# Kernel tuning notes

Hardware: AMD Instinct MI355X
Metric: run time of the kernel (lower is better)

Reference implementation:

```python
import jax, jax.numpy as jnp
import numpy as np

N = 50000        # nodes
E = 250000       # edges (first N are self-loops -> every node has in-degree >= 1)
H = 12           # num_heads
D = 64           # per-head dim (in_dim == out_dim == 64)
NEG_SLOPE = 0.2  # LeakyReLU alpha


def setup_inputs() -> dict:
    key = jax.random.key(0)
    k1, k2, k3, k4, k5, k6, k7 = jax.random.split(key, 7)
    h = jax.random.normal(k1, (N, H * D), dtype=jnp.float32)
    # self-loops + random in-neighbors so segment softmax is well defined for all dst
    src = jnp.concatenate([jnp.arange(N, dtype=jnp.int32),
                           jax.random.randint(k2, (E - N,), 0, N, dtype=jnp.int32)])
    dst = jnp.concatenate([jnp.arange(N, dtype=jnp.int32),
                           jax.random.randint(k3, (E - N,), 0, N, dtype=jnp.int32)])
    xav = 1.414 / np.sqrt(D)  # ~ xavier_normal gain=1.414
    W_fc = jax.random.normal(k4, (D, D), dtype=jnp.float32) * xav
    attn_l = jax.random.normal(k5, (H, D), dtype=jnp.float32) * 0.15
    attn_r = jax.random.normal(k6, (H, D), dtype=jnp.float32) * 0.15
    W_res = jax.random.normal(k7, (D, D), dtype=jnp.float32) * xav
    return {"h": h, "W_fc": W_fc, "attn_l": attn_l, "attn_r": attn_r,
            "W_res": W_res, "src": src, "dst": dst}


def reference(h, W_fc, attn_l, attn_r, W_res, src, dst):
    n = h.shape[0]
    hh = h.reshape(n, H, D)                              # [N,H,D]
    # fc is Linear(D, D, bias=False) shared across heads: y = x @ W^T
    ft = jnp.einsum('nhd,ed->nhe', hh, W_fc)             # [N,H,D]
    a1 = jnp.einsum('nhd,hd->nh', ft, attn_l)            # [N,H]
    a2 = jnp.einsum('nhd,hd->nh', ft, attn_r)            # [N,H]
    # edge_attention: leaky_relu(src.a1 + dst.a2)
    e = jax.nn.leaky_relu(a1[src] + a2[dst], negative_slope=NEG_SLOPE)  # [E,H]
    # segment softmax over incoming edges per destination node (stable)
    m = jax.ops.segment_max(e, dst, num_segments=n)       # [N,H]
    ee = jnp.exp(e - m[dst])                              # [E,H]
    denom = jax.ops.segment_sum(ee, dst, num_segments=n)  # [N,H]
    alpha = ee / denom[dst]                               # [E,H]
    # message: alpha * src ft, scatter-sum into dst
    agg = jax.ops.segment_sum(alpha[:, :, None] * ft[src], dst, num_segments=n)  # [N,H,D]
    # residual: res_fc(h) per head, then ReLU(flatten)
    res = jnp.einsum('nhd,ed->nhe', hh, W_res)            # [N,H,D]
    return jax.nn.relu((res + agg).reshape(n, H * D))     # [N,768]
```

## Files before the change

### kernel.cpp

```cpp
#include <hip/hip_runtime.h>
#include <hip/hip_bf16.h>

#define N_NODES 50000
#define N_EDGES 250000
#define NHEAD   12
#define NH      (N_NODES * NHEAD)
#define ROW_TILES (NH / 16)

typedef __bf16 bf16_t;
typedef __bf16 bf16x8 __attribute__((ext_vector_type(8)));
typedef __bf16 bf16x4 __attribute__((ext_vector_type(4)));
typedef float  f32x4  __attribute__((ext_vector_type(4)));

__device__ __forceinline__ bf16x8 cvt8(f32x4 a, f32x4 b) {
    bf16x8 r;
    r[0] = (bf16_t)a[0]; r[1] = (bf16_t)a[1]; r[2] = (bf16_t)a[2]; r[3] = (bf16_t)a[3];
    r[4] = (bf16_t)b[0]; r[5] = (bf16_t)b[1]; r[6] = (bf16_t)b[2]; r[7] = (bf16_t)b[3];
    return r;
}

__global__ __launch_bounds__(256) void k_deg_prep(
    const int* __restrict__ dst, int* __restrict__ deg,
    const float* __restrict__ wfc, const float* __restrict__ wres,
    const float* __restrict__ attl, const float* __restrict__ attr,
    bf16_t* __restrict__ wfb, bf16_t* __restrict__ wrb,
    bf16_t* __restrict__ ulb, bf16_t* __restrict__ urb)
{
    int b = blockIdx.x;
    if (b < 245) {
        int i4 = b * 256 + threadIdx.x;
        if (i4 < N_EDGES / 4) {
            int4 q = reinterpret_cast<const int4*>(dst)[i4];
            atomicAdd(&deg[q.x], 1);
            atomicAdd(&deg[q.y], 1);
            atomicAdd(&deg[q.z], 1);
            atomicAdd(&deg[q.w], 1);
        }
    } else if (b < 261) {
        int t = (b - 245) * 256 + threadIdx.x;
        wfb[t] = (bf16_t)wfc[t];
        wrb[t] = (bf16_t)wres[t];
    } else if (b < 265) {
        int u = (b - 261) * 256 + threadIdx.x;
        int hh = u >> 6, d = u & 63;
        float s = 0.f;
        if (hh < NHEAD) {
#pragma unroll 8
            for (int e = 0; e < 64; ++e) s += attl[hh * 64 + e] * wfc[e * 64 + d];
        }
        ulb[u] = (bf16_t)s;
    } else {
        int u = (b - 265) * 256 + threadIdx.x;
        int hh = u >> 6, d = u & 63;
        float s = 0.f;
        if (hh < NHEAD) {
#pragma unroll 8
            for (int e = 0; e < 64; ++e) s += attr[hh * 64 + e] * wfc[e * 64 + d];
        }
        urb[u] = (bf16_t)s;
    }
}

__global__ __launch_bounds__(1024) void k_scan(const int* __restrict__ deg,
                                               int* __restrict__ cursor) {
    __shared__ int s[1024];
    const int CH = 52;
    int t = threadIdx.x;
    int base = t * CH;
    int loc[CH];
    if (base + CH <= N_NODES) {
        const int4* p = reinterpret_cast<const int4*>(deg + base);
#pragma unroll
        for (int i = 0; i < CH / 4; ++i) {
            int4 q = p[i];
            loc[4 * i + 0] = q.x; loc[4 * i + 1] = q.y;
            loc[4 * i + 2] = q.z; loc[4 * i + 3] = q.w;
        }
    } else {
#pragma unroll
        for (int i = 0; i < CH; ++i) {
            int idx = base + i;
            loc[i] = (idx < N_NODES) ? deg[idx] : 0;
        }
    }
    int sum = 0;
#pragma unroll
    for (int i = 0; i < CH; ++i) sum += loc[i];
    s[t] = sum;
    __syncthreads();
    for (int off = 1; off < 1024; off <<= 1) {
        int v = (t >= off) ? s[t - off] : 0;
        __syncthreads();
        s[t] += v;
        __syncthreads();
    }
    int run = s[t] - sum;
#pragma unroll
    for (int i = 0; i < CH; ++i) {
        int idx = base + i;
        if (idx < N_NODES) {
            cursor[idx] = run;
            run += loc[i];
        }
    }
}

__global__ __launch_bounds__(256) void k_fill_gemm(
    const int* __restrict__ src, const int* __restrict__ dst,
    int* __restrict__ cursor, int* __restrict__ csr_src,
    const float* __restrict__ h,
    const bf16_t* __restrict__ wfb,
    const bf16_t* __restrict__ wrb,
    const bf16_t* __restrict__ ulb,
    const bf16_t* __restrict__ urb,
    bf16_t* __restrict__ ft,
    bf16_t* __restrict__ resb,
    float* __restrict__ al,
    float* __restrict__ ar)
{
    __shared__ bf16_t sb[4][2][16 * 72];
    if (blockIdx.x >= 1875) {
        int i = (blockIdx.x - 1875) * 256 + threadIdx.x;
        if (i < N_EDGES) {
            int d = dst[i];
            int pos = atomicAdd(&cursor[d], 1);
            csr_src[pos] = src[i];
        }
        return;
    }
    int bid  = blockIdx.x;
    int wv   = threadIdx.x >> 6;
    int lane = threadIdx.x & 63;
    int lr = lane & 15, lg = lane >> 4;
    int l8 = lane & 7,  lrow = lane >> 3;
    bf16_t* fs = &sb[wv][0][0];
    bf16_t* rs = &sb[wv][1][0];

    const f32x4*  hv  = reinterpret_cast<const f32x4*>(h);
    const bf16x8* wf  = reinterpret_cast<const bf16x8*>(wfb);
    const bf16x8* wr  = reinterpret_cast<const bf16x8*>(wrb);
    const bf16x8* ulv = reinterpret_cast<const bf16x8*>(ulb);
    const bf16x8* urv = reinterpret_cast<const bf16x8*>(urb);
    bf16x8 ul0 = ulv[lr * 8 + lg], ul1 = ulv[lr * 8 + 4 + lg];
    bf16x8 ur0 = urv[lr * 8 + lg], ur1 = urv[lr * 8 + 4 + lg];

    const int nw = 1875 * 4;
    int tile = bid * 4 + wv;

    f32x4 c0, c1, c2, c3;
    if (tile < ROW_TILES) {
        int ab = (tile * 16 + lr) * 16 + lg * 2;
        c0 = __builtin_nontemporal_load(hv + ab);
        c1 = __builtin_nontemporal_load(hv + ab + 1);
        c2 = __builtin_nontemporal_load(hv + ab + 8);
        c3 = __builtin_nontemporal_load(hv + ab + 9);
    }
    while (tile < ROW_TILES) {
        int nxt = tile + nw;
        f32x4 n0, n1, n2, n3;
        if (nxt < ROW_TILES) {
            int ab = (nxt * 16 + lr) * 16 + lg * 2;
            n0 = __builtin_nontemporal_load(hv + ab);
            n1 = __builtin_nontemporal_load(hv + ab + 1);
            n2 = __builtin_nontemporal_load(hv + ab + 8);
            n3 = __builtin_nontemporal_load(hv + ab + 9);
        }
        bf16x8 a0 = cvt8(c0, c1), a1 = cvt8(c2, c3);
        int r0 = tile << 4;
        int r  = r0 + lr;
        int hh = r % NHEAD;

        f32x4 dl = {0.f, 0.f, 0.f, 0.f}, dr = {0.f, 0.f, 0.f, 0.f};
        dl = __builtin_amdgcn_mfma_f32_16x16x32_bf16(ul0, a0, dl, 0, 0, 0);
        dl = __builtin_amdgcn_mfma_f32_16x16x32_bf16(ul1, a1, dl, 0, 0, 0);
        dr = __builtin_amdgcn_mfma_f32_16x16x32_bf16(ur0, a0, dr, 0, 0, 0);
        dr = __builtin_amdgcn_mfma_f32_16x16x32_bf16(ur1, a1, dr, 0, 0, 0);
        if (lg == (hh >> 2)) {
#pragma unroll
            for (int j = 0; j < 4; ++j)
                if ((hh & 3) == j) { al[r] = dl[j]; ar[r] = dr[j]; }
        }

#pragma unroll
        for (int nt = 0; nt < 4; ++nt) {
            int brow = (nt * 16 + lr) * 8;
            f32x4 z = {0.f, 0.f, 0.f, 0.f};
            z = __builtin_amdgcn_mfma_f32_16x16x32_bf16(wf[brow + lg],     a0, z, 0, 0, 0);
            z = __builtin_amdgcn_mfma_f32_16x16x32_bf16(wf[brow + 4 + lg], a1, z, 0, 0, 0);
            f32x4 y = {0.f, 0.f, 0.f, 0.f};
            y = __builtin_amdgcn_mfma_f32_16x16x32_bf16(wr[brow + lg],     a0, y, 0, 0, 0);
            y = __builtin_amdgcn_mfma_f32_16x16x32_bf16(wr[brow + 4 + lg], a1, y, 0, 0, 0);
            bf16x4 pf, pe;
#pragma unroll
            for (int j = 0; j < 4; ++j) { pf[j] = (bf16_t)z[j]; pe[j] = (bf16_t)y[j]; }
            *reinterpret_cast<bf16x4*>(fs + lr * 72 + nt * 16 + lg * 4) = pf;
            *reinterpret_cast<bf16x4*>(rs + lr * 72 + nt * 16 + lg * 4) = pe;
        }

#pragma unroll
        for (int k = 0; k < 2; ++k) {
            int row = lrow + k * 8;
            bf16x8 vf = *reinterpret_cast<const bf16x8*>(fs + row * 72 + l8 * 8);
            bf16x8 vr = *reinterpret_cast<const bf16x8*>(rs + row * 72 + l8 * 8);
            *reinterpret_cast<bf16x8*>(ft   + (r0 + row) * 64 + l8 * 8) = vf;
            *reinterpret_cast<bf16x8*>(resb + (r0 + row) * 64 + l8 * 8) = vr;
        }

        c0 = n0; c1 = n1; c2 = n2; c3 = n3;
        tile = nxt;
    }
}

#define DB 8
__global__ __launch_bounds__(256) void k_agg(
    const int* __restrict__ cur, const int* __restrict__ csr_src,
    const float* __restrict__ al, const float* __restrict__ ar,
    const bf16_t* __restrict__ ft, const bf16_t* __restrict__ resb,
    float* __restrict__ out)
{
    int d0 = (blockIdx.x * 256 + threadIdx.x) >> 6;
    d0 = __builtin_amdgcn_readfirstlane(d0);
    if (d0 >= N_NODES) return;
    int l  = threadIdx.x & 63;
    int hA = l >> 3;
    int hB = 8 + (l >> 4);
    int u_l = l / 12;
    int h_l = l - u_l * 12;
    int beg = d0 ? cur[d0 - 1] : 0;
    int end = cur[d0];
    float arW = 0.f;
    if (l < 48) arW = ar[d0 * NHEAD + h_l];

    float accA[8] = {0,0,0,0,0,0,0,0};
    float accB[4] = {0,0,0,0};
    float denA = 0.f, denB = 0.f;

    for (int j0 = beg; j0 < end; j0 += DB) {
        int idx[DB];
#pragma unroll
        for (int u = 0; u < DB; ++u) {
            int j = j0 + u;
            idx[u] = csr_src[(j < end) ? j : beg];
        }
        float wv0 = 0.f, wv1 = 0.f;
        {
            int e0 = idx[0], e1 = idx[4];
            e0 = (u_l == 1) ? idx[1] : e0;  e1 = (u_l == 1) ? idx[5] : e1;
            e0 = (u_l == 2) ? idx[2] : e0;  e1 = (u_l == 2) ? idx[6] : e1;
            e0 = (u_l == 3) ? idx[3] : e0;  e1 = (u_l == 3) ? idx[7] : e1;
            if (l < 48) {
                float x0 = al[e0 * NHEAD + h_l] + arW;
                float x1 = al[e1 * NHEAD + h_l] + arW;
                x0 = (x0 > 0.f) ? x0 : 0.2f * x0;
                x1 = (x1 > 0.f) ? x1 : 0.2f * x1;
                wv0 = ((j0 + u_l)     < end) ? __expf(x0) : 0.f;
                wv1 = ((j0 + 4 + u_l) < end) ? __expf(x1) : 0.f;
            }
        }
        float wA[DB], wB[DB];
#pragma unroll
        for (int u = 0; u < 4; ++u) {
            wA[u]     = __shfl(wv0, u * 12 + hA, 64);
            wB[u]     = __shfl(wv0, u * 12 + hB, 64);
            wA[u + 4] = __shfl(wv1, u * 12 + hA, 64);
            wB[u + 4] = __shfl(wv1, u * 12 + hB, 64);
        }
        bf16x8 vA[DB]; bf16x4 vB[DB];
#pragma unroll
        for (int u = 0; u < DB; ++u) {
            const bf16_t* row = ft + idx[u] * 768;
            vA[u] = *reinterpret_cast<const bf16x8*>(row + 8 * l);
            vB[u] = *reinterpret_cast<const bf16x4*>(row + 512 + 4 * l);
        }
#pragma unroll
        for (int u = 0; u < DB; ++u) {
            denA += wA[u]; denB += wB[u];
#pragma unroll
            for (int k = 0; k < 8; ++k) accA[k] += wA[u] * (float)vA[u][k];
#pragma unroll
            for (int k = 0; k < 4; ++k) accB[k] += wB[u] * (float)vB[u][k];
        }
    }

    const bf16_t* rrow = resb + d0 * 768;
    bf16x8 rA = __builtin_nontemporal_load(reinterpret_cast<const bf16x8*>(rrow + 8 * l));
    bf16x4 rB = __builtin_nontemporal_load(reinterpret_cast<const bf16x4*>(rrow + 512 + 4 * l));
    float* orow = out + d0 * 768;
    f32x4 o0, o1, o2;
    float ia = 1.f / denA, ib = 1.f / denB;
#pragma unroll
    for (int k = 0; k < 4; ++k) {
        float x = (float)rA[k] + accA[k] * ia;         o0[k] = x > 0.f ? x : 0.f;
        float y = (float)rA[k + 4] + accA[k + 4] * ia; o1[k] = y > 0.f ? y : 0.f;
        float z = (float)rB[k] + accB[k] * ib;         o2[k] = z > 0.f ? z : 0.f;
    }
    __builtin_nontemporal_store(o0, reinterpret_cast<f32x4*>(orow + 8 * l));
    __builtin_nontemporal_store(o1, reinterpret_cast<f32x4*>(orow + 8 * l + 4));
    __builtin_nontemporal_store(o2, reinterpret_cast<f32x4*>(orow + 512 + 4 * l));
}

extern "C" void kernel_launch(void* const* d_in, const int* in_sizes, int n_in,
                              void* d_out, int out_size, void* d_ws, size_t ws_size,
                              hipStream_t stream) {
    const float* h    = (const float*)d_in[0];
    const float* wfc  = (const float*)d_in[1];
    const float* attl = (const float*)d_in[2];
    const float* attr = (const float*)d_in[3];
    const float* wres = (const float*)d_in[4];
    const int*   src  = (const int*)d_in[5];
    const int*   dst  = (const int*)d_in[6];
    float* out = (float*)d_out;

    char* ws = (char*)d_ws;
    bf16_t* ft     = (bf16_t*)(ws + 0);
    bf16_t* resb   = (bf16_t*)(ws + 76800000);
    float*  al     = (float*)(ws + 153600000);
    float*  ar     = (float*)(ws + 156000000);
    int*    deg    = (int*)(ws + 158400000);
    int*    cursor = (int*)(ws + 158800896);
    int*    csrsrc = (int*)(ws + 159001344);
    bf16_t* wfb    = (bf16_t*)(ws + 160001344);
    bf16_t* wrb    = (bf16_t*)(ws + 160009536);
    bf16_t* ulb    = (bf16_t*)(ws + 160017728);
    bf16_t* urb    = (bf16_t*)(ws + 160019776);

    (void)hipMemsetAsync(deg, 0, N_NODES * sizeof(int), stream);
    k_deg_prep<<<269, 256, 0, stream>>>(dst, deg, wfc, wres, attl, attr, wfb, wrb, ulb, urb);
    k_scan<<<1, 1024, 0, stream>>>(deg, cursor);
    k_fill_gemm<<<1875 + 977, 256, 0, stream>>>(src, dst, cursor, csrsrc,
                                                h, wfb, wrb, ulb, urb, ft, resb, al, ar);
    k_agg<<<(N_NODES + 3) / 4, 256, 0, stream>>>(cursor, csrsrc, al, ar, ft, resb, out);
}
```

Baseline: 209.6 us.

## Interleave fill and GEMM blocks and deepen h prefetch to two tiles

The CSR fill blocks are now interleaved with GEMM blocks (every third block id) instead of all running after the GEMM blocks, so the atomic scatter overlaps with the streaming GEMM. The GEMM block count changes, and the register prefetch of h goes from one tile ahead to two. Nontemporal loads become ordinary loads. This aims to hide memory latency and balance work across CUs, at the cost of more live registers and a different cache policy for h.

```diff
diff --git a/kernel.cpp b/kernel.cpp
--- a/kernel.cpp
+++ b/kernel.cpp
@@ -6,6 +6,8 @@
 #define NHEAD   12
 #define NH      (N_NODES * NHEAD)
 #define ROW_TILES (NH / 16)
+#define NGEMMB  1954
+#define NFILLB  977
 
 typedef __bf16 bf16_t;
 typedef __bf16 bf16x8 __attribute__((ext_vector_type(8)));
@@ -119,8 +121,9 @@
     float* __restrict__ ar)
 {
     __shared__ bf16_t sb[4][2][16 * 72];
-    if (blockIdx.x >= 1875) {
-        int i = (blockIdx.x - 1875) * 256 + threadIdx.x;
+    int bid = blockIdx.x;
+    if (bid % 3 == 2) {
+        int i = (bid / 3) * 256 + threadIdx.x;
         if (i < N_EDGES) {
             int d = dst[i];
             int pos = atomicAdd(&cursor[d], 1);
@@ -128,7 +131,7 @@
         }
         return;
     }
-    int bid  = blockIdx.x;
+    int gid  = (bid / 3) * 2 + (bid % 3);
     int wv   = threadIdx.x >> 6;
     int lane = threadIdx.x & 63;
     int lr = lane & 15, lg = lane >> 4;
@@ -144,26 +147,28 @@
     bf16x8 ul0 = ulv[lr * 8 + lg], ul1 = ulv[lr * 8 + 4 + lg];
     bf16x8 ur0 = urv[lr * 8 + lg], ur1 = urv[lr * 8 + 4 + lg];
 
-    const int nw = 1875 * 4;
-    int tile = bid * 4 + wv;
-
-    f32x4 c0, c1, c2, c3;
+    const int nw = NGEMMB * 4;
+    int tile = gid * 4 + wv;
+    int t1 = tile + nw;
+
+    f32x4 c0, c1, c2, c3, d0_, d1_, d2_, d3_;
     if (tile < ROW_TILES) {
         int ab = (tile * 16 + lr) * 16 + lg * 2;
-        c0 = __builtin_nontemporal_load(hv + ab);
-        c1 = __builtin_nontemporal_load(hv + ab + 1);
-        c2 = __builtin_nontemporal_load(hv + ab + 8);
-        c3 = __builtin_nontemporal_load(hv + ab + 9);
+        c0 = hv[ab];     c1 = hv[ab + 1];
+        c2 = hv[ab + 8]; c3 = hv[ab + 9];
+    }
+    if (t1 < ROW_TILES) {
+        int ab = (t1 * 16 + lr) * 16 + lg * 2;
+        d0_ = hv[ab];     d1_ = hv[ab + 1];
+        d2_ = hv[ab + 8]; d3_ = hv[ab + 9];
     }
     while (tile < ROW_TILES) {
-        int nxt = tile + nw;
-        f32x4 n0, n1, n2, n3;
-        if (nxt < ROW_TILES) {
-            int ab = (nxt * 16 + lr) * 16 + lg * 2;
-            n0 = __builtin_nontemporal_load(hv + ab);
-            n1 = __builtin_nontemporal_load(hv + ab + 1);
-            n2 = __builtin_nontemporal_load(hv + ab + 8);
-            n3 = __builtin_nontemporal_load(hv + ab + 9);
+        int t2 = t1 + nw;
+        f32x4 e0, e1, e2, e3;
+        if (t2 < ROW_TILES) {
+            int ab = (t2 * 16 + lr) * 16 + lg * 2;
+            e0 = hv[ab];     e1 = hv[ab + 1];
+            e2 = hv[ab + 8]; e3 = hv[ab + 9];
         }
         bf16x8 a0 = cvt8(c0, c1), a1 = cvt8(c2, c3);
         int r0 = tile << 4;
@@ -206,8 +211,9 @@
             *reinterpret_cast<bf16x8*>(resb + (r0 + row) * 64 + l8 * 8) = vr;
         }
 
-        c0 = n0; c1 = n1; c2 = n2; c3 = n3;
-        tile = nxt;
+        c0 = d0_; c1 = d1_; c2 = d2_; c3 = d3_;
+        d0_ = e0; d1_ = e1; d2_ = e2; d3_ = e3;
+        tile = t1; t1 = t2;
     }
 }
 
@@ -327,7 +333,7 @@
     (void)hipMemsetAsync(deg, 0, N_NODES * sizeof(int), stream);
     k_deg_prep<<<269, 256, 0, stream>>>(dst, deg, wfc, wres, attl, attr, wfb, wrb, ulb, urb);
     k_scan<<<1, 1024, 0, stream>>>(deg, cursor);
-    k_fill_gemm<<<1875 + 977, 256, 0, stream>>>(src, dst, cursor, csrsrc,
-                                                h, wfb, wrb, ulb, urb, ft, resb, al, ar);
+    k_fill_gemm<<<NGEMMB + NFILLB, 256, 0, stream>>>(src, dst, cursor, csrsrc,
+                                                     h, wfb, wrb, ulb, urb, ft, resb, al, ar);
     k_agg<<<(N_NODES + 3) / 4, 256, 0, stream>>>(cursor, csrsrc, al, ar, ft, resb, out);
 }
```

Measured after the change: 211.5 us. Within noise of the previous version (+0.9%).

## Replace LDS transpose with wave shuffles and interleave fill/GEMM blocks

Applied to the files above, without the earlier changes.

The GEMM epilogue no longer stages ft/res tiles through shared memory. It transposes the MFMA output across lanes with __shfl and writes each row directly as 16-byte stores. Block IDs are interleaved so every third block runs the CSR fill while the rest run GEMM tiles, and the GEMM block count rises to 1954. This removes LDS traffic and lets the atomic-heavy fill overlap with the bandwidth-bound GEMM, at the cost of extra shuffle and select instructions.

```diff
diff --git a/kernel.cpp b/kernel.cpp
--- a/kernel.cpp
+++ b/kernel.cpp
@@ -6,6 +6,8 @@
 #define NHEAD   12
 #define NH      (N_NODES * NHEAD)
 #define ROW_TILES (NH / 16)
+#define NGEMMB  1954
+#define NFILLB  977
 
 typedef __bf16 bf16_t;
 typedef __bf16 bf16x8 __attribute__((ext_vector_type(8)));
@@ -17,6 +19,33 @@
     r[0] = (bf16_t)a[0]; r[1] = (bf16_t)a[1]; r[2] = (bf16_t)a[2]; r[3] = (bf16_t)a[3];
     r[4] = (bf16_t)b[0]; r[5] = (bf16_t)b[1]; r[6] = (bf16_t)b[2]; r[7] = (bf16_t)b[3];
     return r;
+}
+
+__device__ __forceinline__ uint2 pack4(f32x4 z) {
+    bf16x4 p;
+    p[0] = (bf16_t)z[0]; p[1] = (bf16_t)z[1]; p[2] = (bf16_t)z[2]; p[3] = (bf16_t)z[3];
+    union { bf16x4 b; uint2 u; } c; c.b = p;
+    return c.u;
+}
+
+__device__ __forceinline__ void xpose4(uint2 c0, uint2 c1, uint2 c2, uint2 c3,
+                                       int lr, int lg,
+                                       uint2& g0, uint2& g1, uint2& g2, uint2& g3) {
+    g0 = g1 = g2 = g3 = make_uint2(0, 0);
+#pragma unroll
+    for (int k = 0; k < 4; ++k) {
+        int sel = (lg - k) & 3;
+        uint2 P = (sel == 0) ? c0 : (sel == 1) ? c1 : (sel == 2) ? c2 : c3;
+        int srcl = lr + 16 * ((lg + k) & 3);
+        uint2 R;
+        R.x = (unsigned)__shfl((int)P.x, srcl, 64);
+        R.y = (unsigned)__shfl((int)P.y, srcl, 64);
+        int m = (lg + k) & 3;
+        g0 = (m == 0) ? R : g0;
+        g1 = (m == 1) ? R : g1;
+        g2 = (m == 2) ? R : g2;
+        g3 = (m == 3) ? R : g3;
+    }
 }
 
 __global__ __launch_bounds__(256) void k_deg_prep(
@@ -118,9 +147,9 @@
     float* __restrict__ al,
     float* __restrict__ ar)
 {
-    __shared__ bf16_t sb[4][2][16 * 72];
-    if (blockIdx.x >= 1875) {
-        int i = (blockIdx.x - 1875) * 256 + threadIdx.x;
+    int bid = blockIdx.x;
+    if (bid % 3 == 2) {
+        int i = (bid / 3) * 256 + threadIdx.x;
         if (i < N_EDGES) {
             int d = dst[i];
             int pos = atomicAdd(&cursor[d], 1);
@@ -128,13 +157,10 @@
         }
         return;
     }
-    int bid  = blockIdx.x;
+    int gid  = (bid / 3) * 2 + (bid % 3);
     int wv   = threadIdx.x >> 6;
     int lane = threadIdx.x & 63;
     int lr = lane & 15, lg = lane >> 4;
-    int l8 = lane & 7,  lrow = lane >> 3;
-    bf16_t* fs = &sb[wv][0][0];
-    bf16_t* rs = &sb[wv][1][0];
 
     const f32x4*  hv  = reinterpret_cast<const f32x4*>(h);
     const bf16x8* wf  = reinterpret_cast<const bf16x8*>(wfb);
@@ -144,8 +170,8 @@
     bf16x8 ul0 = ulv[lr * 8 + lg], ul1 = ulv[lr * 8 + 4 + lg];
     bf16x8 ur0 = urv[lr * 8 + lg], ur1 = urv[lr * 8 + 4 + lg];
 
-    const int nw = 1875 * 4;
-    int tile = bid * 4 + wv;
+    const int nw = NGEMMB * 4;
+    int tile = gid * 4 + wv;
 
     f32x4 c0, c1, c2, c3;
     if (tile < ROW_TILES) {
@@ -181,6 +207,7 @@
                 if ((hh & 3) == j) { al[r] = dl[j]; ar[r] = dr[j]; }
         }
 
+        uint2 pf[4], pe[4];
 #pragma unroll
         for (int nt = 0; nt < 4; ++nt) {
             int brow = (nt * 16 + lr) * 8;
@@ -190,21 +217,21 @@
             f32x4 y = {0.f, 0.f, 0.f, 0.f};
             y = __builtin_amdgcn_mfma_f32_16x16x32_bf16(wr[brow + lg],     a0, y, 0, 0, 0);
             y = __builtin_amdgcn_mfma_f32_16x16x32_bf16(wr[brow + 4 + lg], a1, y, 0, 0, 0);
-            bf16x4 pf, pe;
-#pragma unroll
-            for (int j = 0; j < 4; ++j) { pf[j] = (bf16_t)z[j]; pe[j] = (bf16_t)y[j]; }
-            *reinterpret_cast<bf16x4*>(fs + lr * 72 + nt * 16 + lg * 4) = pf;
-            *reinterpret_cast<bf16x4*>(rs + lr * 72 + nt * 16 + lg * 4) = pe;
-        }
-
-#pragma unroll
-        for (int k = 0; k < 2; ++k) {
-            int row = lrow + k * 8;
-            bf16x8 vf = *reinterpret_cast<const bf16x8*>(fs + row * 72 + l8 * 8);
-            bf16x8 vr = *reinterpret_cast<const bf16x8*>(rs + row * 72 + l8 * 8);
-            *reinterpret_cast<bf16x8*>(ft   + (r0 + row) * 64 + l8 * 8) = vf;
-            *reinterpret_cast<bf16x8*>(resb + (r0 + row) * 64 + l8 * 8) = vr;
-        }
+            pf[nt] = pack4(z);
+            pe[nt] = pack4(y);
+        }
+
+        uint2 f0, f1, f2, f3, e0, e1, e2, e3;
+        xpose4(pf[0], pf[1], pf[2], pf[3], lr, lg, f0, f1, f2, f3);
+        xpose4(pe[0], pe[1], pe[2], pe[3], lr, lg, e0, e1, e2, e3);
+        uint4 flo = make_uint4(f0.x, f0.y, f1.x, f1.y);
+        uint4 fhi = make_uint4(f2.x, f2.y, f3.x, f3.y);
+        uint4 elo = make_uint4(e0.x, e0.y, e1.x, e1.y);
+        uint4 ehi = make_uint4(e2.x, e2.y, e3.x, e3.y);
+        *reinterpret_cast<uint4*>(ft   + r * 64 + lg * 16)     = flo;
+        *reinterpret_cast<uint4*>(ft   + r * 64 + lg * 16 + 8) = fhi;
+        *reinterpret_cast<uint4*>(resb + r * 64 + lg * 16)     = elo;
+        *reinterpret_cast<uint4*>(resb + r * 64 + lg * 16 + 8) = ehi;
 
         c0 = n0; c1 = n1; c2 = n2; c3 = n3;
         tile = nxt;
@@ -327,7 +354,7 @@
     (void)hipMemsetAsync(deg, 0, N_NODES * sizeof(int), stream);
     k_deg_prep<<<269, 256, 0, stream>>>(dst, deg, wfc, wres, attl, attr, wfb, wrb, ulb, urb);
     k_scan<<<1, 1024, 0, stream>>>(deg, cursor);
-    k_fill_gemm<<<1875 + 977, 256, 0, stream>>>(src, dst, cursor, csrsrc,
-                                                h, wfb, wrb, ulb, urb, ft, resb, al, ar);
+    k_fill_gemm<<<NGEMMB + NFILLB, 256, 0, stream>>>(src, dst, cursor, csrsrc,
+                                                     h, wfb, wrb, ulb, urb, ft, resb, al, ar);
     k_agg<<<(N_NODES + 3) / 4, 256, 0, stream>>>(cursor, csrsrc, al, ar, ft, resb, out);
 }
```

Result: slower. 223.2 us (+6.5%).
